# Kernel optimization log

Hardware: AMD Instinct MI355X
Metric: run time of the kernel (lower is better)

The kernel has to match this reference:

```python
import jax, jax.numpy as jnp
import numpy as np

DIM = 512
NUM_HEADS = 8
SCALE = (DIM // NUM_HEADS) ** -0.5  # 0.125, per head_dim**-0.5 in source


def setup_inputs() -> dict:
    key = jax.random.key(0)
    k1, k2, k3, k4, k5 = jax.random.split(key, 5)
    B, N, M, C = 4, 4096, 4096, DIM
    x = jax.random.normal(k1, (B, N, C), dtype=jnp.float32)
    support = jax.random.normal(k2, (B, M, C), dtype=jnp.float32)
    attn_mask = jnp.ones((M,), dtype=jnp.int32)
    # params (torch Linear: y = x @ W.T + b); v_linear has no bias (qkv_bias=False)
    Wv = jax.random.normal(k3, (C, C), dtype=jnp.float32) * (1.0 / np.sqrt(C))
    Wp = jax.random.normal(k4, (C, C), dtype=jnp.float32) * (1.0 / np.sqrt(C))
    bp = jax.random.normal(k5, (C,), dtype=jnp.float32) * 0.01
    return {"x": x, "support": support, "attn_mask": attn_mask,
            "Wv": Wv, "Wp": Wp, "bp": bp}


def reference(x, support, attn_mask, Wv, Wp, bp):
    B, N, C = x.shape
    q = jnp.einsum('bnc,dc->bnd', x, Wv)        # v_linear(x)
    k = jnp.einsum('bmc,dc->bmd', support, Wv)  # v_linear(support)
    v = k
    attn = jnp.einsum('bnd,bmd->bnm', q, k) * SCALE
    # DropKey is a no-op in eval / p=0
    attn = jax.nn.softmax(attn, axis=-1)
    # post-softmax key masking: attn[:, :, mask == 0] = 0
    attn = jnp.where(attn_mask[None, None, :] == 0, 0.0, attn)
    out = jnp.einsum('bnm,bmc->bnc', attn, v)   # [B, N, C]
    # faithful to source: transpose(1,2) then flat reshape back to (B, N, C)
    out = jnp.transpose(out, (0, 2, 1)).reshape(B, N, C)
    out = jnp.einsum('bnc,dc->bnd', out, Wp) + bp
    return out
```

## Files before the change

kernel.cpp:

```cpp
#include <hip/hip_runtime.h>

typedef short v8s __attribute__((ext_vector_type(8)));
typedef float v4f __attribute__((ext_vector_type(4)));

#define AS1 __attribute__((address_space(1)))
#define AS3 __attribute__((address_space(3)))

__device__ __forceinline__ void gload_lds16(const void* g, void* l) {
  __builtin_amdgcn_global_load_lds((const AS1 unsigned*)g, (AS3 unsigned*)l, 16, 0, 0);
}

__device__ __forceinline__ unsigned short f2bf(float f) {
  union { float f; unsigned u; } x; x.f = f;
  unsigned r = x.u + 0x7fffu + ((x.u >> 16) & 1u);
  return (unsigned short)(r >> 16);
}

__device__ __forceinline__ unsigned cvtpk(float lo, float hi) {
  unsigned r;
  asm("v_cvt_pk_bf16_f32 %0, %1, %2" : "=v"(r) : "v"(lo), "v"(hi));
  return r;
}

#define MF(B, A, C) __builtin_amdgcn_mfma_f32_16x16x32_bf16((B), (A), (C), 0, 0, 0)

template <int MODE>
__launch_bounds__(256)
__global__ void gemm_p_kernel(const float* __restrict__ A0f,
                              const float* __restrict__ A1f,
                              const unsigned short* __restrict__ Abf,
                              const float* __restrict__ Wsrc,
                              const int* __restrict__ amask,
                              unsigned short* __restrict__ Cb,
                              unsigned short* __restrict__ KT,
                              const float* __restrict__ bias,
                              float* __restrict__ Cf) {
  __shared__ __align__(16) char smem[66048];
  constexpr int ABUF = (MODE == 0) ? 16384 : 8192;
  constexpr int BSTRIDE = ABUF + 16384;
  const int tid = threadIdx.x;
  const int wave = tid >> 6, lane = tid & 63, lr = lane & 15, lg = lane >> 4;
  const int mb = blockIdx.x >> 2, nb = blockIdx.x & 3;
  const int wr = wave >> 1, wc = wave & 1;

  v4f acc[4][4];
#pragma unroll
  for (int i = 0; i < 4; ++i)
#pragma unroll
    for (int j = 0; j < 4; ++j) acc[i][j] = (v4f){0.f, 0.f, 0.f, 0.f};

  const int f32slot = ((lane & 7) ^ (lane >> 3)) << 4;
  const char* wSrc = (const char*)Wsrc +
      (size_t)(nb * 128 + (lane >> 3)) * 2048 + f32slot;
  const char* aSrcF = nullptr;
  const char* aSrcB = nullptr;
  if constexpr (MODE == 0) {
    aSrcF = (mb < 128)
        ? (const char*)A0f + ((size_t)mb * 128 + (lane >> 3)) * 2048 + f32slot
        : (const char*)A1f + ((size_t)(mb - 128) * 128 + (lane >> 3)) * 2048 + f32slot;
  } else {
    aSrcB = (const char*)Abf +
        ((size_t)mb * 128 + wave * 32 + (lane >> 2)) * 1024 +
        ((((lane & 3) ^ ((lane >> 3) & 3))) << 4);
  }

  auto stageTo = [&](int buf, int kt) {
    char* bA = &smem[buf * BSTRIDE];
    char* bW = bA + ABUF;
    if constexpr (MODE == 0) {
      const char* s = aSrcF + (size_t)kt * 128;
#pragma unroll
      for (int i = 0; i < 4; ++i)
        gload_lds16(s + (size_t)(i * 32 + wave * 8) * 2048, bA + i * 4096 + wave * 1024);
    } else {
      const char* s = aSrcB + (size_t)kt * 64;
      gload_lds16(s, bA + wave * 2048);
      gload_lds16(s + (size_t)16 * 1024, bA + wave * 2048 + 1024);
    }
    const char* s2 = wSrc + (size_t)kt * 128;
#pragma unroll
    for (int i = 0; i < 4; ++i)
      gload_lds16(s2 + (size_t)(i * 32 + wave * 8) * 2048, bW + i * 4096 + wave * 1024);
  };

  auto rdcvt = [&](const char* base, int row) -> v8s {
    const int sw = row & 7;
    v4f f0 = *(const v4f*)(base + row * 128 + (((lg * 2) ^ sw) << 4));
    v4f f1 = *(const v4f*)(base + row * 128 + (((lg * 2 + 1) ^ sw) << 4));
    union { unsigned u[4]; v8s v; } r;
    r.u[0] = cvtpk(f0[0], f0[1]);
    r.u[1] = cvtpk(f0[2], f0[3]);
    r.u[2] = cvtpk(f1[0], f1[1]);
    r.u[3] = cvtpk(f1[2], f1[3]);
    return r.v;
  };

  stageTo(0, 0);
  __syncthreads();
  int buf = 0;

  for (int kt = 0; kt < 16; ++kt) {
    if (kt + 1 < 16) stageTo(buf ^ 1, kt + 1);

    const char* bA = &smem[buf * BSTRIDE];
    const char* bW = bA + ABUF;
    v8s af[4], bfr[4];
    if constexpr (MODE == 0) {
#pragma unroll
      for (int mi = 0; mi < 4; ++mi) af[mi] = rdcvt(bA, wr * 64 + mi * 16 + lr);
    } else {
      const int fo = (lg * 16) ^ (((lr >> 1) & 3) << 4);
#pragma unroll
      for (int mi = 0; mi < 4; ++mi)
        af[mi] = *(const v8s*)&bA[(wr * 64 + mi * 16 + lr) * 64 + fo];
    }
#pragma unroll
    for (int ni = 0; ni < 4; ++ni) bfr[ni] = rdcvt(bW, wc * 64 + ni * 16 + lr);
#pragma unroll
    for (int mi = 0; mi < 4; ++mi)
#pragma unroll
      for (int ni = 0; ni < 4; ++ni)
        acc[mi][ni] = MF(bfr[ni], af[mi], acc[mi][ni]);

    __syncthreads();
    buf ^= 1;
  }

  if constexpr (MODE == 0) {
    const float sc = (mb < 128) ? 0.125f : 1.0f;
    const bool isK = (mb >= 128);
    const int mg0 = isK ? ((mb - 128) & 31) * 128 : 0;
    int* mlds = (int*)&smem[65536];
    if (isK && tid < 128) mlds[tid] = amask[mg0 + tid];
#pragma unroll
    for (int mi = 0; mi < 4; ++mi) {
      const int ml = wr * 64 + mi * 16 + lr;
#pragma unroll
      for (int ni = 0; ni < 4; ++ni) {
        const int nl = wc * 64 + ni * 16 + lg * 4;
        ushort4 pk;
        pk.x = f2bf(acc[mi][ni][0] * sc);
        pk.y = f2bf(acc[mi][ni][1] * sc);
        pk.z = f2bf(acc[mi][ni][2] * sc);
        pk.w = f2bf(acc[mi][ni][3] * sc);
        *(ushort4*)&smem[ml * 256 + ((nl * 2) ^ ((ml & 7) << 4))] = pk;
      }
    }
    __syncthreads();
#pragma unroll
    for (int p = 0; p < 8; ++p) {
      const int row = p * 16 + (tid >> 4);
      const int off = (tid & 15) * 16;
      v8s v = *(const v8s*)&smem[row * 256 + (off ^ ((row & 7) << 4))];
      *(v8s*)(Cb + ((size_t)mb * 128 + row) * 512 + nb * 128 + (tid & 15) * 8) = v;
    }
    if (isK) {
      const int bb = (mb - 128) >> 5;
      unsigned short* KTb = KT + ((size_t)bb * 512 + nb * 128) * 4096 + mg0;
#pragma unroll
      for (int p = 0; p < 8; ++p) {
        const int u = p * 256 + tid;
        const int c = u & 127, mc = u >> 7;
        union { unsigned short a[8]; v8s v; } vals;
#pragma unroll
        for (int j = 0; j < 8; ++j) {
          const int m = mc * 8 + j;
          unsigned short s =
              *(const unsigned short*)&smem[m * 256 + (((c >> 3) ^ j) << 4) + (c & 7) * 2];
          vals.a[j] = mlds[m] ? s : (unsigned short)0;
        }
        *(v8s*)(KTb + (size_t)c * 4096 + mc * 8) = vals.v;
      }
    }
  } else {
#pragma unroll
    for (int mi = 0; mi < 4; ++mi) {
      const int ml = wr * 64 + mi * 16 + lr;
#pragma unroll
      for (int ni = 0; ni < 4; ++ni) {
        const int nl = wc * 64 + ni * 16 + lg * 4;
        *(float4*)&smem[ml * 512 + ((nl * 4) ^ ((ml & 7) << 4))] =
            (float4){acc[mi][ni][0], acc[mi][ni][1], acc[mi][ni][2], acc[mi][ni][3]};
      }
    }
    __syncthreads();
    const float4 bb4 = *(const float4*)(bias + nb * 128 + (tid & 31) * 4);
#pragma unroll
    for (int p = 0; p < 16; ++p) {
      const int row = p * 8 + (tid >> 5);
      const int off = (tid & 31) * 16;
      float4 v = *(const float4*)&smem[row * 512 + (off ^ ((row & 7) << 4))];
      v.x += bb4.x; v.y += bb4.y; v.z += bb4.z; v.w += bb4.w;
      *(float4*)(Cf + ((size_t)mb * 128 + row) * 512 + nb * 128 + (tid & 31) * 4) = v;
    }
  }
}

__launch_bounds__(256)
__global__ void gemm_s_kernel(const unsigned short* __restrict__ A,
                              const unsigned short* __restrict__ W,
                              unsigned short* __restrict__ C,
                              int nbTot,
                              long long sbA, long long sbW, long long sbC) {
  __shared__ __align__(16) char smem[65536];
  const int tid = threadIdx.x;
  const int wave = tid >> 6, lane = tid & 63, lr = lane & 15, lg = lane >> 4;
  const int cpx = gridDim.x >> 3;
  const int swz = (blockIdx.x & 7) * cpx + (blockIdx.x >> 3);
  const int batch = swz / nbTot;
  const int rem = swz - batch * nbTot;
  const int g = rem >> 7, sr = rem & 127;
  const int mb = (g >> 1) * 8 + (sr & 7);
  const int nb = (g & 1) * 16 + (sr >> 3);
  const unsigned short* Ab = A + (size_t)batch * sbA;
  const unsigned short* Wb = W + (size_t)batch * sbW;
  unsigned short* Cb = C + (size_t)batch * sbC;
  const int wr = wave >> 1, wc = wave & 1;

  v4f acc[4][4];
#pragma unroll
  for (int i = 0; i < 4; ++i)
#pragma unroll
    for (int j = 0; j < 4; ++j) acc[i][j] = (v4f){0.f, 0.f, 0.f, 0.f};

  const int r8 = tid >> 3;
  const int srcSlot = ((tid & 7) ^ (r8 & 7)) << 4;
  const char* aSrc = (const char*)Ab + ((size_t)(mb * 128 + r8)) * 1024 + srcSlot;
  const char* wSrc = (const char*)Wb + ((size_t)(nb * 128 + r8)) * 1024 + srcSlot;

  auto stageTo = [&](int buf, int kt) {
    const int ko = kt * 128;
    char* bA = &smem[buf * 32768];
    char* bW = bA + 16384;
#pragma unroll
    for (int i = 0; i < 4; ++i)
      gload_lds16(aSrc + i * 32 * 1024 + ko, bA + i * 4096 + tid * 16);
#pragma unroll
    for (int i = 0; i < 4; ++i)
      gload_lds16(wSrc + i * 32 * 1024 + ko, bW + i * 4096 + tid * 16);
  };

  auto rd = [&](const char* b, int row, int sub) -> v8s {
    return *(const v8s*)&b[row * 128 + (((sub * 4 + lg) ^ (row & 7)) << 4)];
  };

  stageTo(0, 0);
  __syncthreads();

#pragma unroll
  for (int kt = 0; kt < 8; ++kt) {
    const int buf = kt & 1;
    if (kt + 1 < 8) stageTo(buf ^ 1, kt + 1);

    const char* bA = &smem[buf * 32768];
    const char* bW = bA + 16384;
#pragma unroll
    for (int sub = 0; sub < 2; ++sub) {
      v8s af[4], bfr[4];
#pragma unroll
      for (int mi = 0; mi < 4; ++mi) af[mi] = rd(bA, wr * 64 + mi * 16 + lr, sub);
#pragma unroll
      for (int ni = 0; ni < 4; ++ni) bfr[ni] = rd(bW, wc * 64 + ni * 16 + lr, sub);
#pragma unroll
      for (int mi = 0; mi < 4; ++mi)
#pragma unroll
        for (int ni = 0; ni < 4; ++ni)
          acc[mi][ni] = MF(bfr[ni], af[mi], acc[mi][ni]);
    }

    __syncthreads();
  }

#pragma unroll
  for (int mi = 0; mi < 4; ++mi) {
    const int ml = wr * 64 + mi * 16 + lr;
#pragma unroll
    for (int ni = 0; ni < 4; ++ni) {
      const int nl = wc * 64 + ni * 16 + lg * 4;
      ushort4 pk;
      pk.x = f2bf(__expf(acc[mi][ni][0]));
      pk.y = f2bf(__expf(acc[mi][ni][1]));
      pk.z = f2bf(__expf(acc[mi][ni][2]));
      pk.w = f2bf(__expf(acc[mi][ni][3]));
      *(ushort4*)&smem[ml * 256 + ((nl * 2) ^ ((ml & 7) << 4))] = pk;
    }
  }
  __syncthreads();
#pragma unroll
  for (int p = 0; p < 8; ++p) {
    const int row = p * 16 + (tid >> 4);
    const int off = (tid & 15) * 16;
    v8s v = *(const v8s*)&smem[row * 256 + (off ^ ((row & 7) << 4))];
    *(v8s*)(Cb + ((size_t)mb * 128 + row) * 4096 + (size_t)nb * 128 + (tid & 15) * 8) = v;
  }
}

__launch_bounds__(512)
__global__ void gemm_ot_kernel(const unsigned short* __restrict__ A,
                               const unsigned short* __restrict__ W,
                               unsigned short* __restrict__ C,
                               int nbTot, long long sbA, long long sbW,
                               long long sbC) {
  __shared__ __align__(16) char smem[98816];
  float* psum_sh = (float*)&smem[98304];
  const int t = threadIdx.x;
  const int wave = t >> 6, lane = t & 63, lr = lane & 15, lg = lane >> 4;
  const int wr = wave >> 1, wc = wave & 1;
  const int cpx = gridDim.x >> 3;
  const int swz = (blockIdx.x & 7) * cpx + (blockIdx.x >> 3);
  const int batch = swz / nbTot;
  const int rem = swz - batch * nbTot;
  const int nb = rem >> 1, mb = rem & 1;
  const unsigned short* Ab = A + (size_t)batch * sbA;
  const unsigned short* Wb = W + (size_t)batch * sbW;
  unsigned short* Cb = C + (size_t)batch * sbC;

  v4f acc[4][4];
#pragma unroll
  for (int i = 0; i < 4; ++i)
#pragma unroll
    for (int j = 0; j < 4; ++j) acc[i][j] = (v4f){0.f, 0.f, 0.f, 0.f};
  v4f accs[4];
#pragma unroll
  for (int i = 0; i < 4; ++i) accs[i] = (v4f){0.f, 0.f, 0.f, 0.f};
  const v8s ones = (v8s){0x3F80, 0x3F80, 0x3F80, 0x3F80,
                         0x3F80, 0x3F80, 0x3F80, 0x3F80};

  const int r8 = t >> 3;
  const int srcSlot = ((t & 7) ^ (r8 & 7)) << 4;
  const char* aSrc = (const char*)Ab + ((size_t)(mb * 256 + r8)) * 8192 + srcSlot;
  const char* wSrc = (const char*)Wb + ((size_t)(nb * 128 + r8)) * 8192 + srcSlot;

  auto stageTo = [&](int buf, int kt) {
    const size_t ko = (size_t)kt * 128;
    char* base = &smem[buf * 49152];
#pragma unroll
    for (int i = 0; i < 4; ++i)
      gload_lds16(aSrc + (size_t)(i * 64) * 8192 + ko, base + i * 8192 + t * 16);
#pragma unroll
    for (int i = 0; i < 2; ++i)
      gload_lds16(wSrc + (size_t)(i * 64) * 8192 + ko, base + 32768 + i * 8192 + t * 16);
  };

  auto rd = [&](const char* b, int row, int sub) -> v8s {
    return *(const v8s*)&b[row * 128 + (((sub * 4 + lg) ^ (row & 7)) << 4)];
  };

  stageTo(0, 0);
  __syncthreads();
  int buf = 0;

  for (int kt = 0; kt < 64; ++kt) {
    if (kt + 1 < 64) stageTo(buf ^ 1, kt + 1);

    const char* bA = &smem[buf * 49152];
    const char* bW = bA + 32768;
#pragma unroll
    for (int sub = 0; sub < 2; ++sub) {
      v8s af[4], bfr[4];
#pragma unroll
      for (int mi = 0; mi < 4; ++mi) af[mi] = rd(bA, wr * 64 + mi * 16 + lr, sub);
#pragma unroll
      for (int ni = 0; ni < 4; ++ni) bfr[ni] = rd(bW, wc * 64 + ni * 16 + lr, sub);
#pragma unroll
      for (int mi = 0; mi < 4; ++mi)
#pragma unroll
        for (int ni = 0; ni < 4; ++ni)
          acc[mi][ni] = MF(bfr[ni], af[mi], acc[mi][ni]);
#pragma unroll
      for (int ni = 0; ni < 4; ++ni) accs[ni] = MF(ones, bfr[ni], accs[ni]);
    }

    __syncthreads();
    buf ^= 1;
  }

  if (wr == 0 && lg == 0) {
#pragma unroll
    for (int ni = 0; ni < 4; ++ni)
      psum_sh[wc * 64 + ni * 16 + lr] = accs[ni][0];
  }
  __syncthreads();
  v4f inv4[4];
#pragma unroll
  for (int ni = 0; ni < 4; ++ni) {
    const float4 l4 = *(const float4*)&psum_sh[wc * 64 + ni * 16 + lg * 4];
    inv4[ni] = (v4f){1.0f / l4.x, 1.0f / l4.y, 1.0f / l4.z, 1.0f / l4.w};
  }

#pragma unroll
  for (int mi = 0; mi < 4; ++mi) {
    const int ml = wr * 64 + mi * 16 + lr;
#pragma unroll
    for (int ni = 0; ni < 4; ++ni) {
      const int nl = wc * 64 + ni * 16 + lg * 4;
      ushort4 pk;
      pk.x = f2bf(acc[mi][ni][0] * inv4[ni][0]);
      pk.y = f2bf(acc[mi][ni][1] * inv4[ni][1]);
      pk.z = f2bf(acc[mi][ni][2] * inv4[ni][2]);
      pk.w = f2bf(acc[mi][ni][3] * inv4[ni][3]);
      *(ushort4*)&smem[ml * 256 + ((nl * 2) ^ ((ml & 7) << 4))] = pk;
    }
  }
  __syncthreads();
#pragma unroll
  for (int p = 0; p < 8; ++p) {
    const int row = p * 32 + (t >> 4);
    const int off = (t & 15) * 16;
    v8s v = *(const v8s*)&smem[row * 256 + (off ^ ((row & 7) << 4))];
    *(v8s*)(Cb + ((size_t)mb * 256 + row) * 4096 + nb * 128 + (t & 15) * 8) = v;
  }
}

extern "C" void kernel_launch(void* const* d_in, const int* in_sizes, int n_in,
                              void* d_out, int out_size, void* d_ws, size_t ws_size,
                              hipStream_t stream) {
  (void)in_sizes; (void)n_in; (void)out_size;
  const float* x = (const float*)d_in[0];
  const float* sup = (const float*)d_in[1];
  const int* amask = (const int*)d_in[2];
  const float* Wv = (const float*)d_in[3];
  const float* Wp = (const float*)d_in[4];
  const float* bp = (const float*)d_in[5];
  float* out = (float*)d_out;

  char* ws = (char*)d_ws;
  unsigned short* QKb = (unsigned short*)ws;
  unsigned short* KT = (unsigned short*)(ws + (size_t)33554432);
  unsigned short* OTb = (unsigned short*)(ws + (size_t)50331648);
  unsigned short* S = (unsigned short*)(ws + (size_t)67108864);
  unsigned short* Qb = QKb;
  unsigned short* Kb = QKb + (size_t)16384 * 512;

  const long long QS = (long long)4096 * 512;
  const long long SS = (long long)4096 * 4096;
  const long long OS = (long long)512 * 4096;

  gemm_p_kernel<0><<<dim3(1024), dim3(256), 0, stream>>>(
      x, sup, nullptr, Wv, amask, QKb, KT, nullptr, nullptr);

  if (ws_size >= (size_t)201326592) {
    gemm_s_kernel<<<dim3(4096), dim3(256), 0, stream>>>(
        Qb, Kb, S, 1024, QS, QS, SS);
    gemm_ot_kernel<<<dim3(256), dim3(512), 0, stream>>>(
        KT, S, OTb, 64, OS, SS, OS);
  } else {
    for (int b = 0; b < 4; ++b) {
      gemm_s_kernel<<<dim3(1024), dim3(256), 0, stream>>>(
          Qb + (size_t)b * QS, Kb + (size_t)b * QS, S, 1024, 0, 0, 0);
      gemm_ot_kernel<<<dim3(64), dim3(512), 0, stream>>>(
          KT + (size_t)b * OS, S, OTb + (size_t)b * OS, 64, 0, 0, 0);
    }
  }
  gemm_p_kernel<1><<<dim3(512), dim3(256), 0, stream>>>(
      nullptr, nullptr, OTb, Wp, nullptr, nullptr, nullptr, bp, out);
}
```

Measured before the change: 239.1 us.

## Stage fp32 operands through registers and convert to bf16 before LDS

The GEMM kernel now loads fp32 A/W tiles into registers, converts them to bf16 once, and writes bf16 into swizzled LDS, instead of copying fp32 directly to LDS and converting on every fragment read. The K tile doubles to 64 elements over 8 iterations, each with two MFMA sub-steps, and the next tile's global loads are issued before compute with their LDS writes after. This removes redundant per-wave conversions and halves LDS footprint per element, at the cost of more registers for staging and losing the asynchronous global-to-LDS path for the fp32 operands.

```diff
diff --git a/kernel.cpp b/kernel.cpp
--- a/kernel.cpp
+++ b/kernel.cpp
@@ -36,8 +36,6 @@
                               const float* __restrict__ bias,
                               float* __restrict__ Cf) {
   __shared__ __align__(16) char smem[66048];
-  constexpr int ABUF = (MODE == 0) ? 16384 : 8192;
-  constexpr int BSTRIDE = ABUF + 16384;
   const int tid = threadIdx.x;
   const int wave = tid >> 6, lane = tid & 63, lr = lane & 15, lg = lane >> 4;
   const int mb = blockIdx.x >> 2, nb = blockIdx.x & 3;
@@ -49,81 +47,108 @@
 #pragma unroll
     for (int j = 0; j < 4; ++j) acc[i][j] = (v4f){0.f, 0.f, 0.f, 0.f};
 
-  const int f32slot = ((lane & 7) ^ (lane >> 3)) << 4;
-  const char* wSrc = (const char*)Wsrc +
-      (size_t)(nb * 128 + (lane >> 3)) * 2048 + f32slot;
-  const char* aSrcF = nullptr;
+  const int srow = tid >> 3;
+  const int sslot = tid & 7;
+  const int wswz = (sslot ^ (srow & 7)) << 4;
+
+  const float* wS = Wsrc + (size_t)(nb * 128 + srow) * 512 + sslot * 8;
+  const float* aS = nullptr;
   const char* aSrcB = nullptr;
   if constexpr (MODE == 0) {
-    aSrcF = (mb < 128)
-        ? (const char*)A0f + ((size_t)mb * 128 + (lane >> 3)) * 2048 + f32slot
-        : (const char*)A1f + ((size_t)(mb - 128) * 128 + (lane >> 3)) * 2048 + f32slot;
+    aS = (mb < 128)
+        ? A0f + (size_t)(mb * 128 + srow) * 512 + sslot * 8
+        : A1f + (size_t)((mb - 128) * 128 + srow) * 512 + sslot * 8;
   } else {
-    aSrcB = (const char*)Abf +
-        ((size_t)mb * 128 + wave * 32 + (lane >> 2)) * 1024 +
-        ((((lane & 3) ^ ((lane >> 3) & 3))) << 4);
-  }
-
-  auto stageTo = [&](int buf, int kt) {
-    char* bA = &smem[buf * BSTRIDE];
-    char* bW = bA + ABUF;
-    if constexpr (MODE == 0) {
-      const char* s = aSrcF + (size_t)kt * 128;
-#pragma unroll
-      for (int i = 0; i < 4; ++i)
-        gload_lds16(s + (size_t)(i * 32 + wave * 8) * 2048, bA + i * 4096 + wave * 1024);
-    } else {
-      const char* s = aSrcB + (size_t)kt * 64;
-      gload_lds16(s, bA + wave * 2048);
-      gload_lds16(s + (size_t)16 * 1024, bA + wave * 2048 + 1024);
-    }
-    const char* s2 = wSrc + (size_t)kt * 128;
+    aSrcB = (const char*)Abf + (size_t)(mb * 128 + srow) * 1024 + wswz;
+  }
+
+  v4f ra[8], rw[8];
+  auto loadW = [&](int kt) {
+#pragma unroll
+    for (int u = 0; u < 4; ++u) {
+      const float* p = wS + (size_t)(u * 32) * 512 + kt * 64;
+      rw[2 * u] = *(const v4f*)p;
+      rw[2 * u + 1] = *(const v4f*)(p + 4);
+    }
+  };
+  auto writeW = [&](int buf) {
+    char* bW = &smem[buf * 32768 + 16384];
+#pragma unroll
+    for (int u = 0; u < 4; ++u) {
+      union { unsigned q[4]; v8s v; } d;
+      d.q[0] = cvtpk(rw[2 * u][0], rw[2 * u][1]);
+      d.q[1] = cvtpk(rw[2 * u][2], rw[2 * u][3]);
+      d.q[2] = cvtpk(rw[2 * u + 1][0], rw[2 * u + 1][1]);
+      d.q[3] = cvtpk(rw[2 * u + 1][2], rw[2 * u + 1][3]);
+      *(v8s*)&bW[(u * 32 + srow) * 128 + wswz] = d.v;
+    }
+  };
+  auto loadA = [&](int kt) {
+#pragma unroll
+    for (int u = 0; u < 4; ++u) {
+      const float* p = aS + (size_t)(u * 32) * 512 + kt * 64;
+      ra[2 * u] = *(const v4f*)p;
+      ra[2 * u + 1] = *(const v4f*)(p + 4);
+    }
+  };
+  auto writeA = [&](int buf) {
+    char* bA = &smem[buf * 32768];
+#pragma unroll
+    for (int u = 0; u < 4; ++u) {
+      union { unsigned q[4]; v8s v; } d;
+      d.q[0] = cvtpk(ra[2 * u][0], ra[2 * u][1]);
+      d.q[1] = cvtpk(ra[2 * u][2], ra[2 * u][3]);
+      d.q[2] = cvtpk(ra[2 * u + 1][0], ra[2 * u + 1][1]);
+      d.q[3] = cvtpk(ra[2 * u + 1][2], ra[2 * u + 1][3]);
+      *(v8s*)&bA[(u * 32 + srow) * 128 + wswz] = d.v;
+    }
+  };
+  auto stageA_lds = [&](int buf, int kt) {
+    const char* s = aSrcB + kt * 128;
+    char* bA = &smem[buf * 32768];
 #pragma unroll
     for (int i = 0; i < 4; ++i)
-      gload_lds16(s2 + (size_t)(i * 32 + wave * 8) * 2048, bW + i * 4096 + wave * 1024);
-  };
-
-  auto rdcvt = [&](const char* base, int row) -> v8s {
-    const int sw = row & 7;
-    v4f f0 = *(const v4f*)(base + row * 128 + (((lg * 2) ^ sw) << 4));
-    v4f f1 = *(const v4f*)(base + row * 128 + (((lg * 2 + 1) ^ sw) << 4));
-    union { unsigned u[4]; v8s v; } r;
-    r.u[0] = cvtpk(f0[0], f0[1]);
-    r.u[1] = cvtpk(f0[2], f0[3]);
-    r.u[2] = cvtpk(f1[0], f1[1]);
-    r.u[3] = cvtpk(f1[2], f1[3]);
-    return r.v;
-  };
-
-  stageTo(0, 0);
-  __syncthreads();
-  int buf = 0;
-
-  for (int kt = 0; kt < 16; ++kt) {
-    if (kt + 1 < 16) stageTo(buf ^ 1, kt + 1);
-
-    const char* bA = &smem[buf * BSTRIDE];
-    const char* bW = bA + ABUF;
-    v8s af[4], bfr[4];
-    if constexpr (MODE == 0) {
-#pragma unroll
-      for (int mi = 0; mi < 4; ++mi) af[mi] = rdcvt(bA, wr * 64 + mi * 16 + lr);
-    } else {
-      const int fo = (lg * 16) ^ (((lr >> 1) & 3) << 4);
+      gload_lds16(s + (size_t)(i * 32) * 1024, bA + i * 4096 + tid * 16);
+  };
+
+  auto rd = [&](const char* b, int row, int sub) -> v8s {
+    return *(const v8s*)&b[row * 128 + (((sub * 4 + lg) ^ (row & 7)) << 4)];
+  };
+
+  if constexpr (MODE == 0) { loadA(0); } else { stageA_lds(0, 0); }
+  loadW(0);
+  if constexpr (MODE == 0) writeA(0);
+  writeW(0);
+  __syncthreads();
+
+#pragma unroll
+  for (int kt = 0; kt < 8; ++kt) {
+    const int buf = kt & 1;
+    const bool more = (kt + 1 < 8);
+    if (more) {
+      if constexpr (MODE == 0) loadA(kt + 1); else stageA_lds(buf ^ 1, kt + 1);
+      loadW(kt + 1);
+    }
+    const char* bA = &smem[buf * 32768];
+    const char* bW = bA + 16384;
+#pragma unroll
+    for (int sub = 0; sub < 2; ++sub) {
+      v8s af[4], bfr[4];
+#pragma unroll
+      for (int mi = 0; mi < 4; ++mi) af[mi] = rd(bA, wr * 64 + mi * 16 + lr, sub);
+#pragma unroll
+      for (int ni = 0; ni < 4; ++ni) bfr[ni] = rd(bW, wc * 64 + ni * 16 + lr, sub);
 #pragma unroll
       for (int mi = 0; mi < 4; ++mi)
-        af[mi] = *(const v8s*)&bA[(wr * 64 + mi * 16 + lr) * 64 + fo];
-    }
-#pragma unroll
-    for (int ni = 0; ni < 4; ++ni) bfr[ni] = rdcvt(bW, wc * 64 + ni * 16 + lr);
-#pragma unroll
-    for (int mi = 0; mi < 4; ++mi)
-#pragma unroll
-      for (int ni = 0; ni < 4; ++ni)
-        acc[mi][ni] = MF(bfr[ni], af[mi], acc[mi][ni]);
-
+#pragma unroll
+        for (int ni = 0; ni < 4; ++ni)
+          acc[mi][ni] = MF(bfr[ni], af[mi], acc[mi][ni]);
+    }
+    if (more) {
+      if constexpr (MODE == 0) writeA(buf ^ 1);
+      writeW(buf ^ 1);
+    }
     __syncthreads();
-    buf ^= 1;
   }
 
   if constexpr (MODE == 0) {
```

Measured after the change: 240.3 us. No clear change (+0.5%).
